# Kernel optimization log

Hardware: AMD Instinct MI355X
Metric: run time of the kernel (lower is better)

Reference implementation:

```python
import jax, jax.numpy as jnp
import numpy as np

N = 50000   # nodes per graph
E = 800000  # edges per graph
D = 128     # in_dim (num_features)
H = 128     # hidden_channels
R = 8       # num_etypes


def setup_inputs() -> dict:
    key = jax.random.key(0)
    ks = jax.random.split(key, 32)
    inp = {}
    inp["x1"] = jax.random.normal(ks[0], (N, D), dtype=jnp.float32)
    inp["edge_index1"] = jax.random.randint(ks[1], (2, E), 0, N)
    inp["edge_type1"] = jnp.sort(jax.random.randint(ks[2], (E,), 0, R))
    inp["x2"] = jax.random.normal(ks[3], (N, D), dtype=jnp.float32)
    inp["edge_index2"] = jax.random.randint(ks[4], (2, E), 0, N)
    inp["edge_type2"] = jnp.sort(jax.random.randint(ks[5], (E,), 0, R))
    # RGCNConv params: relation weights [R, in, out], root weight [in, out], bias [out]
    dims = [(D, H), (H, H), (H, H)]
    k = 6
    for l, (di, do) in enumerate(dims):
        s = 1.0 / np.sqrt(di)
        inp[f"W{l}"] = jax.random.normal(ks[k], (R, di, do), dtype=jnp.float32) * s; k += 1
        inp[f"root{l}"] = jax.random.normal(ks[k], (di, do), dtype=jnp.float32) * s; k += 1
        inp[f"bias{l}"] = jnp.zeros((do,), dtype=jnp.float32)
    # FCL: MLP on concat(u1, u2) of width 2*H -> H -> 1 (assumed architecture)
    s = 1.0 / np.sqrt(2 * H)
    inp["fc1_w"] = jax.random.normal(ks[k], (2 * H, H), dtype=jnp.float32) * s; k += 1
    inp["fc1_b"] = jnp.zeros((H,), dtype=jnp.float32)
    s = 1.0 / np.sqrt(H)
    inp["fc2_w"] = jax.random.normal(ks[k], (H, 1), dtype=jnp.float32) * s; k += 1
    inp["fc2_b"] = jnp.zeros((1,), dtype=jnp.float32)
    return inp


def rgcn_conv(x, src, dst, etype, W, root, bias):
    # PyG RGCNConv: out_i = root @ x_i + bias + sum_r mean_{j in N_r(i)} W_r x_j
    # transform all nodes by all relation weights: [R, N, H]
    t = jnp.einsum('nd,rdh->rnh', x, W)
    msg = t[etype, src]                       # [E, H] per-edge gathered messages
    comb = dst * R + etype                    # combined (node, relation) segment id
    cnt = jax.ops.segment_sum(jnp.ones((E,), x.dtype), comb, num_segments=N * R)
    msg = msg * (1.0 / jnp.maximum(cnt, 1.0))[comb][:, None]  # per-relation mean norm
    agg = jax.ops.segment_sum(msg, dst, num_segments=N)       # scatter-add over relations
    return agg + x @ root + bias


def gnn(x, edge_index, edge_type, params):
    src, dst = edge_index[0], edge_index[1]
    u = jax.nn.relu(rgcn_conv(x, src, dst, edge_type, *params[0]))
    u = jax.nn.relu(rgcn_conv(u, src, dst, edge_type, *params[1]))
    u = rgcn_conv(u, src, dst, edge_type, *params[2])
    return jnp.mean(u, axis=0).reshape(1, -1)  # [1, H]


def reference(x1, edge_index1, edge_type1, x2, edge_index2, edge_type2,
              W0, root0, bias0, W1, root1, bias1, W2, root2, bias2,
              fc1_w, fc1_b, fc2_w, fc2_b):
    params = [(W0, root0, bias0), (W1, root1, bias1), (W2, root2, bias2)]
    u1 = gnn(x1, edge_index1, edge_type1, params)
    u2 = gnn(x2, edge_index2, edge_type2, params)
    h = jnp.concatenate([u1, u2], axis=-1)    # [1, 2H]
    return jax.nn.relu(h @ fc1_w + fc1_b) @ fc2_w + fc2_b  # [1, 1]
```

## Files before the change

kernel.cpp:

```cpp
#include <hip/hip_runtime.h>

#define R_ET 8
#define DH 128

typedef __bf16 bf16x8 __attribute__((ext_vector_type(8)));
typedef float f32x4 __attribute__((ext_vector_type(4)));

__device__ __forceinline__ ushort f2bf(float f) {
  unsigned u = __float_as_uint(f);
  u += 0x7fff + ((u >> 16) & 1);
  return (ushort)(u >> 16);
}


__global__ void count_kernel(const int* __restrict__ ei, const int* __restrict__ et,
                             int* __restrict__ cnt, int E) {
  int e = blockIdx.x * blockDim.x + threadIdx.x;
  if (e < E) atomicAdd(&cnt[ei[E + e] * R_ET + et[e]], 1);
}

__global__ __launch_bounds__(1024) void scan1_kernel(const int* __restrict__ cnt,
                                                     int* __restrict__ off,
                                                     int* __restrict__ bsum, int N) {
  __shared__ int s[1024];
  int tid = threadIdx.x;
  int node = blockIdx.x * 1024 + tid;
  int d = 0;
  if (node < N) {
    const int4* c = (const int4*)&cnt[node * R_ET];
    int4 a = c[0], b = c[1];
    d = a.x + a.y + a.z + a.w + b.x + b.y + b.z + b.w;
  }
  s[tid] = d;
  __syncthreads();
  for (int step = 1; step < 1024; step <<= 1) {
    int v = (tid >= step) ? s[tid - step] : 0;
    __syncthreads();
    s[tid] += v;
    __syncthreads();
  }
  if (node < N) off[node] = s[tid] - d;
  if (tid == 1023) bsum[blockIdx.x] = s[1023];
}

__global__ __launch_bounds__(1024) void scan2_kernel(int* __restrict__ bsum, int nb) {
  __shared__ int s[1024];
  int tid = threadIdx.x;
  int v = (tid < nb) ? bsum[tid] : 0;
  s[tid] = v;
  __syncthreads();
  for (int step = 1; step < 1024; step <<= 1) {
    int x = (tid >= step) ? s[tid - step] : 0;
    __syncthreads();
    s[tid] += x;
    __syncthreads();
  }
  if (tid < nb) bsum[tid] = s[tid] - v;
}

__global__ __launch_bounds__(1024) void scan3_kernel(int* __restrict__ off,
                                                     int* __restrict__ cursor,
                                                     const int* __restrict__ bsum,
                                                     int N, int E) {
  int node = blockIdx.x * 1024 + threadIdx.x;
  if (node < N) {
    int o = off[node] + bsum[blockIdx.x];
    off[node] = o;
    cursor[node] = o;
  }
  if (node == 0) off[N] = E;
}

__global__ void place_kernel(const int* __restrict__ ei, const int* __restrict__ et,
                             const int* __restrict__ cnt, int* __restrict__ cursor,
                             int2* __restrict__ meta, int E) {
  int e = blockIdx.x * blockDim.x + threadIdx.x;
  if (e >= E) return;
  int src = ei[e], dst = ei[E + e], r = et[e];
  int slot = atomicAdd(&cursor[dst], 1);
  meta[slot] = make_int2(src | (r << 28),
                         __float_as_int(1.f / (float)cnt[dst * R_ET + r]));
}

__global__ __launch_bounds__(256) void wconv_kernel(const float* __restrict__ root,
                                                    const float* __restrict__ W,
                                                    ushort* __restrict__ Wt) {
  int mat = blockIdx.x;
  const float* src = (mat == 0) ? root : (W + (size_t)(mat - 1) * DH * DH);
  ushort* dst = Wt + (size_t)mat * DH * DH;
  for (int idx = threadIdx.x; idx < DH * DH; idx += 256) {
    int n = idx >> 7, k = idx & 127;
    dst[n * DH + (((k >> 3) ^ (n & 7)) << 3) + (k & 7)] = f2bf(src[k * DH + n]);
  }
}

__global__ __launch_bounds__(256) void aconv_kernel(const float* __restrict__ src,
                                                    ushort* __restrict__ dst,
                                                    int total, int padtotal) {
  int i4 = (blockIdx.x * 256 + threadIdx.x) * 4;
  if (i4 >= padtotal) return;
  int row = i4 >> 7, k = i4 & 127;
  ushort4 o = make_ushort4(0, 0, 0, 0);
  if (i4 < total) {
    float4 v = *(const float4*)&src[i4];
    o = make_ushort4(f2bf(v.x), f2bf(v.y), f2bf(v.z), f2bf(v.w));
  }
  *(ushort4*)&dst[(size_t)row * DH + (((k >> 3) ^ (row & 7)) << 3) + (k & 7)] = o;
}

__global__ __launch_bounds__(256) void gemm_mfma(
    const ushort* __restrict__ Abf, const ushort* __restrict__ Wt,
    const float* __restrict__ bias, float* __restrict__ y,
    ushort* __restrict__ t, int N) {
  __shared__ ushort As[128 * DH];
  __shared__ ushort Bs[128 * DH];
  const int tid = threadIdx.x;
  const int wave = tid >> 6, lane = tid & 63;
  const int quad = lane >> 4, l15 = lane & 15;
  const int rbase = blockIdx.x * 128;
  const int wr = (wave >> 1) * 64, wc = (wave & 1) * 64;

  const ushort* gA = Abf + (size_t)rbase * DH;
#pragma unroll
  for (int it = 0; it < 8; it++) {
    __builtin_amdgcn_global_load_lds(
        (const __attribute__((address_space(1))) void*)(gA + (it * 256 + tid) * 8),
        (__attribute__((address_space(3))) void*)(As + (it * 256 + wave * 64) * 8), 16, 0, 0);
  }

  for (int m = 0; m < 3; m++) {
    const int mat = blockIdx.y * 3 + m;
    const ushort* gB = Wt + (size_t)mat * DH * DH;
    if (m) __syncthreads();
#pragma unroll
    for (int it = 0; it < 8; it++) {
      __builtin_amdgcn_global_load_lds(
          (const __attribute__((address_space(1))) void*)(gB + (it * 256 + tid) * 8),
          (__attribute__((address_space(3))) void*)(Bs + (it * 256 + wave * 64) * 8), 16, 0, 0);
    }
    __syncthreads();

    f32x4 acc[4][4];
#pragma unroll
    for (int i = 0; i < 4; i++)
#pragma unroll
      for (int j = 0; j < 4; j++) acc[i][j] = (f32x4){0.f, 0.f, 0.f, 0.f};

#pragma unroll
    for (int kc = 0; kc < 4; kc++) {
      bf16x8 af[4], bfr[4];
#pragma unroll
      for (int i = 0; i < 4; i++) {
        int ra = wr + i * 16 + l15;
        int rb = wc + i * 16 + l15;
        af[i] = *(const bf16x8*)&As[ra * DH + (((kc * 4 + quad) ^ (ra & 7)) << 3)];
        bfr[i] = *(const bf16x8*)&Bs[rb * DH + (((kc * 4 + quad) ^ (rb & 7)) << 3)];
      }
#pragma unroll
      for (int i = 0; i < 4; i++)
#pragma unroll
        for (int j = 0; j < 4; j++)
          acc[i][j] = __builtin_amdgcn_mfma_f32_16x16x32_bf16(af[i], bfr[j], acc[i][j], 0, 0, 0);
    }

    if (mat == 0) {
#pragma unroll
      for (int j = 0; j < 4; j++) {
        int col = wc + j * 16 + l15;
        float bv = bias[col];
#pragma unroll
        for (int i = 0; i < 4; i++)
#pragma unroll
          for (int r = 0; r < 4; r++) {
            int row = rbase + wr + i * 16 + quad * 4 + r;
            if (row < N) y[(size_t)row * DH + col] = acc[i][j][r] + bv;
          }
      }
    } else {
      ushort* tp = t + (size_t)(mat - 1) * N * DH;
#pragma unroll
      for (int j = 0; j < 4; j++) {
        int col = wc + j * 16 + l15;
#pragma unroll
        for (int i = 0; i < 4; i++)
#pragma unroll
          for (int r = 0; r < 4; r++) {
            int row = rbase + wr + i * 16 + quad * 4 + r;
            if (row < N) tp[(size_t)row * DH + col] = f2bf(acc[i][j][r]);
          }
      }
    }
  }
}

__device__ __forceinline__ void gather_accum(const int2* __restrict__ meta,
                                             const ushort* __restrict__ t,
                                             int start, int end, int lane, int N,
                                             float& ax, float& ay) {
  const int colb = lane * 2;
  for (int base = start; base < end; base += 64) {
    int m = min(64, end - base);
    int2 md = make_int2(0, 0);
    if (lane < m) md = meta[base + lane];
    int j = 0;
    for (; j + 4 <= m; j += 4) {
      int p0 = __shfl(md.x, j),     q0 = __shfl(md.y, j);
      int p1 = __shfl(md.x, j + 1), q1 = __shfl(md.y, j + 1);
      int p2 = __shfl(md.x, j + 2), q2 = __shfl(md.y, j + 2);
      int p3 = __shfl(md.x, j + 3), q3 = __shfl(md.y, j + 3);
      unsigned u0 = *(const unsigned*)&t[(((size_t)((unsigned)p0 >> 28) * N + (p0 & 0x0fffffff)) << 7) + colb];
      unsigned u1 = *(const unsigned*)&t[(((size_t)((unsigned)p1 >> 28) * N + (p1 & 0x0fffffff)) << 7) + colb];
      unsigned u2 = *(const unsigned*)&t[(((size_t)((unsigned)p2 >> 28) * N + (p2 & 0x0fffffff)) << 7) + colb];
      unsigned u3 = *(const unsigned*)&t[(((size_t)((unsigned)p3 >> 28) * N + (p3 & 0x0fffffff)) << 7) + colb];
      float s0 = __int_as_float(q0), s1 = __int_as_float(q1);
      float s2 = __int_as_float(q2), s3 = __int_as_float(q3);
      ax = fmaf(__uint_as_float(u0 << 16), s0, ax);
      ay = fmaf(__uint_as_float(u0 & 0xffff0000u), s0, ay);
      ax = fmaf(__uint_as_float(u1 << 16), s1, ax);
      ay = fmaf(__uint_as_float(u1 & 0xffff0000u), s1, ay);
      ax = fmaf(__uint_as_float(u2 << 16), s2, ax);
      ay = fmaf(__uint_as_float(u2 & 0xffff0000u), s2, ay);
      ax = fmaf(__uint_as_float(u3 << 16), s3, ax);
      ay = fmaf(__uint_as_float(u3 & 0xffff0000u), s3, ay);
    }
    for (; j < m; j++) {
      int pj = __shfl(md.x, j);
      float sj = __int_as_float(__shfl(md.y, j));
      unsigned u = *(const unsigned*)&t[(((size_t)((unsigned)pj >> 28) * N + (pj & 0x0fffffff)) << 7) + colb];
      ax = fmaf(__uint_as_float(u << 16), sj, ax);
      ay = fmaf(__uint_as_float(u & 0xffff0000u), sj, ay);
    }
  }
}

__global__ __launch_bounds__(256) void gather_mid(
    const int* __restrict__ off, const int2* __restrict__ meta,
    const ushort* __restrict__ t, const float* __restrict__ y,
    ushort* __restrict__ Abf, int N) {
  int dst = blockIdx.x * 4 + (threadIdx.x >> 6);
  if (dst >= N) return;
  int lane = threadIdx.x & 63;
  float ax = 0.f, ay = 0.f;
  gather_accum(meta, t, off[dst], off[dst + 1], lane, N, ax, ay);
  float2 yv = *(const float2*)&y[(size_t)dst * DH + lane * 2];
  float rx = fmaxf(yv.x + ax, 0.f);
  float ry = fmaxf(yv.y + ay, 0.f);
  unsigned o = (unsigned)f2bf(rx) | ((unsigned)f2bf(ry) << 16);
  int k = lane * 2;
  *(unsigned*)&Abf[(size_t)dst * DH + (((k >> 3) ^ (dst & 7)) << 3) + (k & 7)] = o;
}

__global__ __launch_bounds__(256) void gather_last(
    const int* __restrict__ off, const int2* __restrict__ meta,
    const ushort* __restrict__ t, float* __restrict__ y, int N) {
  int dst = blockIdx.x * 4 + (threadIdx.x >> 6);
  if (dst >= N) return;
  int lane = threadIdx.x & 63;
  float ax = 0.f, ay = 0.f;
  gather_accum(meta, t, off[dst], off[dst + 1], lane, N, ax, ay);
  float2* yp = (float2*)&y[(size_t)dst * DH + lane * 2];
  float2 yv = *yp;
  yv.x += ax;
  yv.y += ay;
  *yp = yv;
}

__global__ __launch_bounds__(256) void pool_kernel(const float* __restrict__ y,
                                                   float* __restrict__ u, int N) {
  __shared__ float s[256];
  int tid = threadIdx.x;
  int c = tid & 127, rr = tid >> 7;
  int n0 = blockIdx.x * 100;
  int nend = min(n0 + 100, N);
  float sum = 0.f;
  for (int n = n0 + rr; n < nend; n += 2) sum += y[(size_t)n * DH + c];
  s[tid] = sum;
  __syncthreads();
  if (tid < 128) atomicAdd(&u[c], s[tid] + s[tid + 128]);
}

__global__ __launch_bounds__(256) void mlp_kernel(
    const float* __restrict__ u, const float* __restrict__ fc1w,
    const float* __restrict__ fc1b, const float* __restrict__ fc2w,
    const float* __restrict__ fc2b, float* __restrict__ out, int N) {
  __shared__ float uin[256];
  __shared__ float hred[128];
  int tid = threadIdx.x;
  uin[tid] = u[tid] * (1.f / (float)N);
  __syncthreads();
  if (tid < 128) {
    float s = fc1b[tid];
    for (int i = 0; i < 256; i++) s = fmaf(uin[i], fc1w[i * 128 + tid], s);
    s = fmaxf(s, 0.f);
    hred[tid] = s * fc2w[tid];
  }
  __syncthreads();
  if (tid == 0) {
    float s = fc2b[0];
    for (int i = 0; i < 128; i++) s += hred[i];
    out[0] = s;
  }
}

extern "C" void kernel_launch(void* const* d_in, const int* in_sizes, int n_in,
                              void* d_out, int out_size, void* d_ws, size_t ws_size,
                              hipStream_t stream) {
  const float* x[2] = {(const float*)d_in[0], (const float*)d_in[3]};
  const int* ei[2] = {(const int*)d_in[1], (const int*)d_in[4]};
  const int* et[2] = {(const int*)d_in[2], (const int*)d_in[5]};
  const float* Wp[3] = {(const float*)d_in[6], (const float*)d_in[9], (const float*)d_in[12]};
  const float* rootp[3] = {(const float*)d_in[7], (const float*)d_in[10], (const float*)d_in[13]};
  const float* biasp[3] = {(const float*)d_in[8], (const float*)d_in[11], (const float*)d_in[14]};
  const float* fc1w = (const float*)d_in[15];
  const float* fc1b = (const float*)d_in[16];
  const float* fc2w = (const float*)d_in[17];
  const float* fc2b = (const float*)d_in[18];

  const int N = in_sizes[0] / DH;
  const int E = in_sizes[2];
  const int Npad = (N + 127) & ~127;
  const int NB = (N + 1023) / 1024;

  char* ws = (char*)d_ws;
  size_t ob = 0;
  auto alloc = [&](size_t bytes) {
    void* p = ws + ob;
    ob = (ob + bytes + 255) & ~(size_t)255;
    return p;
  };
  float* y = (float*)alloc((size_t)N * DH * 4);
  int* cnt = (int*)alloc((size_t)N * R_ET * 4);
  int* offs = (int*)alloc((size_t)(N + 1) * 4);
  int* cursor = (int*)alloc((size_t)N * 4);
  int* bsum = (int*)alloc(1024 * 4);
  int2* meta = (int2*)alloc((size_t)E * 8);
  float* u = (float*)alloc(1024);
  ushort* Abf = (ushort*)alloc((size_t)Npad * DH * 2);
  ushort* Wt = (ushort*)alloc((size_t)3 * 9 * DH * DH * 2);
  ushort* tbuf = (ushort*)alloc((size_t)R_ET * N * DH * 2);
  (void)ws_size;

  hipMemsetAsync(u, 0, 2 * DH * sizeof(float), stream);
  for (int l = 0; l < 3; l++)
    wconv_kernel<<<9, 256, 0, stream>>>(rootp[l], Wp[l], Wt + (size_t)l * 9 * DH * DH);

  dim3 ggrid(Npad / 128, 3);
  dim3 egrid((E + 255) / 256);
  dim3 ngrid((N + 3) / 4);
  const int total = N * DH, padtotal = Npad * DH;
  dim3 agrid((padtotal / 4 + 255) / 256);

  for (int g = 0; g < 2; g++) {
    hipMemsetAsync(cnt, 0, (size_t)N * R_ET * sizeof(int), stream);
    count_kernel<<<egrid, 256, 0, stream>>>(ei[g], et[g], cnt, E);
    scan1_kernel<<<NB, 1024, 0, stream>>>(cnt, offs, bsum, N);
    scan2_kernel<<<1, 1024, 0, stream>>>(bsum, NB);
    scan3_kernel<<<NB, 1024, 0, stream>>>(offs, cursor, bsum, N, E);
    place_kernel<<<egrid, 256, 0, stream>>>(ei[g], et[g], cnt, cursor, meta, E);
    aconv_kernel<<<agrid, 256, 0, stream>>>(x[g], Abf, total, padtotal);
    for (int l = 0; l < 3; l++) {
      gemm_mfma<<<ggrid, 256, 0, stream>>>(Abf, Wt + (size_t)l * 9 * DH * DH,
                                           biasp[l], y, tbuf, N);
      if (l < 2) {
        gather_mid<<<ngrid, 256, 0, stream>>>(offs, meta, tbuf, y, Abf, N);
      } else {
        gather_last<<<ngrid, 256, 0, stream>>>(offs, meta, tbuf, y, N);
      }
    }
    pool_kernel<<<(N + 99) / 100, 256, 0, stream>>>(y, u + g * DH, N);
  }
  mlp_kernel<<<1, 256, 0, stream>>>(u, fc1w, fc1b, fc2w, fc2b, (float*)d_out, N);
}
```

Measured before the change: 887.6 us.

## Sort edges by (dst, relation), shrink edge metadata, fuse pooling and staged GEMM stores

The CSR is now built over (node, relation) segments, so per-edge metadata shrinks to a single int. The mean normalization is computed per destination from the counts and broadcast by shuffle. The root transform goes into a ninth bf16 slab instead of an fp32 y buffer. GEMM output is staged through LDS for coalesced 16-byte stores. The final gather fuses mean pooling with atomic adds, which removes the pool kernel and the fp32 y traffic, and the last-layer bias is folded into the MLP. In exchange, the scan now runs over an 8x larger segment array, and the root path is stored in bf16, which adds rounding error.

```diff
diff --git a/kernel.cpp b/kernel.cpp
--- a/kernel.cpp
+++ b/kernel.cpp
@@ -5,6 +5,7 @@
 
 typedef __bf16 bf16x8 __attribute__((ext_vector_type(8)));
 typedef float f32x4 __attribute__((ext_vector_type(4)));
+typedef ushort u16x8 __attribute__((ext_vector_type(8)));
 
 __device__ __forceinline__ ushort f2bf(float f) {
   unsigned u = __float_as_uint(f);
@@ -12,7 +13,6 @@
   return (ushort)(u >> 16);
 }
 
-
 __global__ void count_kernel(const int* __restrict__ ei, const int* __restrict__ et,
                              int* __restrict__ cnt, int E) {
   int e = blockIdx.x * blockDim.x + threadIdx.x;
@@ -21,16 +21,11 @@
 
 __global__ __launch_bounds__(1024) void scan1_kernel(const int* __restrict__ cnt,
                                                      int* __restrict__ off,
-                                                     int* __restrict__ bsum, int N) {
+                                                     int* __restrict__ bsum, int M) {
   __shared__ int s[1024];
   int tid = threadIdx.x;
-  int node = blockIdx.x * 1024 + tid;
-  int d = 0;
-  if (node < N) {
-    const int4* c = (const int4*)&cnt[node * R_ET];
-    int4 a = c[0], b = c[1];
-    d = a.x + a.y + a.z + a.w + b.x + b.y + b.z + b.w;
-  }
+  int i = blockIdx.x * 1024 + tid;
+  int d = (i < M) ? cnt[i] : 0;
   s[tid] = d;
   __syncthreads();
   for (int step = 1; step < 1024; step <<= 1) {
@@ -39,7 +34,7 @@
     s[tid] += v;
     __syncthreads();
   }
-  if (node < N) off[node] = s[tid] - d;
+  if (i < M) off[i] = s[tid] - d;
   if (tid == 1023) bsum[blockIdx.x] = s[1023];
 }
 
@@ -61,32 +56,30 @@
 __global__ __launch_bounds__(1024) void scan3_kernel(int* __restrict__ off,
                                                      int* __restrict__ cursor,
                                                      const int* __restrict__ bsum,
-                                                     int N, int E) {
-  int node = blockIdx.x * 1024 + threadIdx.x;
-  if (node < N) {
-    int o = off[node] + bsum[blockIdx.x];
-    off[node] = o;
-    cursor[node] = o;
-  }
-  if (node == 0) off[N] = E;
+                                                     int M, int E) {
+  int i = blockIdx.x * 1024 + threadIdx.x;
+  if (i < M) {
+    int o = off[i] + bsum[blockIdx.x];
+    off[i] = o;
+    cursor[i] = o;
+  }
+  if (i == 0) off[M] = E;
 }
 
 __global__ void place_kernel(const int* __restrict__ ei, const int* __restrict__ et,
-                             const int* __restrict__ cnt, int* __restrict__ cursor,
-                             int2* __restrict__ meta, int E) {
+                             int* __restrict__ cursor, int* __restrict__ meta, int E) {
   int e = blockIdx.x * blockDim.x + threadIdx.x;
   if (e >= E) return;
   int src = ei[e], dst = ei[E + e], r = et[e];
-  int slot = atomicAdd(&cursor[dst], 1);
-  meta[slot] = make_int2(src | (r << 28),
-                         __float_as_int(1.f / (float)cnt[dst * R_ET + r]));
+  int slot = atomicAdd(&cursor[dst * R_ET + r], 1);
+  meta[slot] = src | (r << 28);
 }
 
 __global__ __launch_bounds__(256) void wconv_kernel(const float* __restrict__ root,
                                                     const float* __restrict__ W,
                                                     ushort* __restrict__ Wt) {
   int mat = blockIdx.x;
-  const float* src = (mat == 0) ? root : (W + (size_t)(mat - 1) * DH * DH);
+  const float* src = (mat == 8) ? root : (W + (size_t)mat * DH * DH);
   ushort* dst = Wt + (size_t)mat * DH * DH;
   for (int idx = threadIdx.x; idx < DH * DH; idx += 256) {
     int n = idx >> 7, k = idx & 127;
@@ -110,8 +103,7 @@
 
 __global__ __launch_bounds__(256) void gemm_mfma(
     const ushort* __restrict__ Abf, const ushort* __restrict__ Wt,
-    const float* __restrict__ bias, float* __restrict__ y,
-    ushort* __restrict__ t, int N) {
+    ushort* __restrict__ t, int Npad) {
   __shared__ ushort As[128 * DH];
   __shared__ ushort Bs[128 * DH];
   const int tid = threadIdx.x;
@@ -163,57 +155,46 @@
           acc[i][j] = __builtin_amdgcn_mfma_f32_16x16x32_bf16(af[i], bfr[j], acc[i][j], 0, 0, 0);
     }
 
-    if (mat == 0) {
+    __syncthreads();
+#pragma unroll
+    for (int i = 0; i < 4; i++)
 #pragma unroll
       for (int j = 0; j < 4; j++) {
         int col = wc + j * 16 + l15;
-        float bv = bias[col];
-#pragma unroll
-        for (int i = 0; i < 4; i++)
-#pragma unroll
-          for (int r = 0; r < 4; r++) {
-            int row = rbase + wr + i * 16 + quad * 4 + r;
-            if (row < N) y[(size_t)row * DH + col] = acc[i][j][r] + bv;
-          }
+#pragma unroll
+        for (int r = 0; r < 4; r++)
+          Bs[(wr + i * 16 + quad * 4 + r) * DH + col] = f2bf(acc[i][j][r]);
       }
-    } else {
-      ushort* tp = t + (size_t)(mat - 1) * N * DH;
-#pragma unroll
-      for (int j = 0; j < 4; j++) {
-        int col = wc + j * 16 + l15;
-#pragma unroll
-        for (int i = 0; i < 4; i++)
-#pragma unroll
-          for (int r = 0; r < 4; r++) {
-            int row = rbase + wr + i * 16 + quad * 4 + r;
-            if (row < N) tp[(size_t)row * DH + col] = f2bf(acc[i][j][r]);
-          }
-      }
-    }
-  }
-}
-
-__device__ __forceinline__ void gather_accum(const int2* __restrict__ meta,
+    __syncthreads();
+    ushort* tp = t + ((size_t)mat * Npad + rbase) * DH;
+#pragma unroll
+    for (int c = 0; c < 8; c++) {
+      u16x8 v = *(const u16x8*)&Bs[tid * 64 + c * 8];
+      *(u16x8*)&tp[tid * 64 + c * 8] = v;
+    }
+  }
+}
+
+__device__ __forceinline__ void gather_accum(const int* __restrict__ meta,
                                              const ushort* __restrict__ t,
-                                             int start, int end, int lane, int N,
+                                             int start, int end, int lane, int colb,
+                                             float invl, int NpadS,
                                              float& ax, float& ay) {
-  const int colb = lane * 2;
   for (int base = start; base < end; base += 64) {
     int m = min(64, end - base);
-    int2 md = make_int2(0, 0);
-    if (lane < m) md = meta[base + lane];
+    int md = (lane < m) ? meta[base + lane] : 0;
     int j = 0;
     for (; j + 4 <= m; j += 4) {
-      int p0 = __shfl(md.x, j),     q0 = __shfl(md.y, j);
-      int p1 = __shfl(md.x, j + 1), q1 = __shfl(md.y, j + 1);
-      int p2 = __shfl(md.x, j + 2), q2 = __shfl(md.y, j + 2);
-      int p3 = __shfl(md.x, j + 3), q3 = __shfl(md.y, j + 3);
-      unsigned u0 = *(const unsigned*)&t[(((size_t)((unsigned)p0 >> 28) * N + (p0 & 0x0fffffff)) << 7) + colb];
-      unsigned u1 = *(const unsigned*)&t[(((size_t)((unsigned)p1 >> 28) * N + (p1 & 0x0fffffff)) << 7) + colb];
-      unsigned u2 = *(const unsigned*)&t[(((size_t)((unsigned)p2 >> 28) * N + (p2 & 0x0fffffff)) << 7) + colb];
-      unsigned u3 = *(const unsigned*)&t[(((size_t)((unsigned)p3 >> 28) * N + (p3 & 0x0fffffff)) << 7) + colb];
-      float s0 = __int_as_float(q0), s1 = __int_as_float(q1);
-      float s2 = __int_as_float(q2), s3 = __int_as_float(q3);
+      int p0 = __shfl(md, j), p1 = __shfl(md, j + 1);
+      int p2 = __shfl(md, j + 2), p3 = __shfl(md, j + 3);
+      int r0 = (unsigned)p0 >> 28, r1 = (unsigned)p1 >> 28;
+      int r2 = (unsigned)p2 >> 28, r3 = (unsigned)p3 >> 28;
+      float s0 = __shfl(invl, r0), s1 = __shfl(invl, r1);
+      float s2 = __shfl(invl, r2), s3 = __shfl(invl, r3);
+      unsigned u0 = *(const unsigned*)&t[r0 * NpadS + ((p0 & 0x0fffffff) << 7) + colb];
+      unsigned u1 = *(const unsigned*)&t[r1 * NpadS + ((p1 & 0x0fffffff) << 7) + colb];
+      unsigned u2 = *(const unsigned*)&t[r2 * NpadS + ((p2 & 0x0fffffff) << 7) + colb];
+      unsigned u3 = *(const unsigned*)&t[r3 * NpadS + ((p3 & 0x0fffffff) << 7) + colb];
       ax = fmaf(__uint_as_float(u0 << 16), s0, ax);
       ay = fmaf(__uint_as_float(u0 & 0xffff0000u), s0, ay);
       ax = fmaf(__uint_as_float(u1 << 16), s1, ax);
@@ -224,9 +205,10 @@
       ay = fmaf(__uint_as_float(u3 & 0xffff0000u), s3, ay);
     }
     for (; j < m; j++) {
-      int pj = __shfl(md.x, j);
-      float sj = __int_as_float(__shfl(md.y, j));
-      unsigned u = *(const unsigned*)&t[(((size_t)((unsigned)pj >> 28) * N + (pj & 0x0fffffff)) << 7) + colb];
+      int pj = __shfl(md, j);
+      int rj = (unsigned)pj >> 28;
+      float sj = __shfl(invl, rj);
+      unsigned u = *(const unsigned*)&t[rj * NpadS + ((pj & 0x0fffffff) << 7) + colb];
       ax = fmaf(__uint_as_float(u << 16), sj, ax);
       ay = fmaf(__uint_as_float(u & 0xffff0000u), sj, ay);
     }
@@ -234,59 +216,64 @@
 }
 
 __global__ __launch_bounds__(256) void gather_mid(
-    const int* __restrict__ off, const int2* __restrict__ meta,
-    const ushort* __restrict__ t, const float* __restrict__ y,
-    ushort* __restrict__ Abf, int N) {
+    const int* __restrict__ off, const int* __restrict__ meta,
+    const int* __restrict__ cnt, const ushort* __restrict__ t,
+    const float* __restrict__ bias, ushort* __restrict__ Abf, int N, int Npad) {
   int dst = blockIdx.x * 4 + (threadIdx.x >> 6);
   if (dst >= N) return;
-  int lane = threadIdx.x & 63;
+  int lane = threadIdx.x & 63, colb = lane * 2;
+  int dst8 = dst * R_ET;
+  int NpadS = Npad * DH;
+  float invl = 1.f / (float)cnt[dst8 + (lane & 7)];
   float ax = 0.f, ay = 0.f;
-  gather_accum(meta, t, off[dst], off[dst + 1], lane, N, ax, ay);
-  float2 yv = *(const float2*)&y[(size_t)dst * DH + lane * 2];
-  float rx = fmaxf(yv.x + ax, 0.f);
-  float ry = fmaxf(yv.y + ay, 0.f);
+  gather_accum(meta, t, off[dst8], off[dst8 + 8], lane, colb, invl, NpadS, ax, ay);
+  unsigned u9 = *(const unsigned*)&t[8 * NpadS + (dst << 7) + colb];
+  float2 bv = *(const float2*)&bias[colb];
+  float rx = fmaxf(__uint_as_float(u9 << 16) + ax + bv.x, 0.f);
+  float ry = fmaxf(__uint_as_float(u9 & 0xffff0000u) + ay + bv.y, 0.f);
   unsigned o = (unsigned)f2bf(rx) | ((unsigned)f2bf(ry) << 16);
-  int k = lane * 2;
-  *(unsigned*)&Abf[(size_t)dst * DH + (((k >> 3) ^ (dst & 7)) << 3) + (k & 7)] = o;
+  *(unsigned*)&Abf[(size_t)dst * DH + (((colb >> 3) ^ (dst & 7)) << 3) + (colb & 7)] = o;
 }
 
 __global__ __launch_bounds__(256) void gather_last(
-    const int* __restrict__ off, const int2* __restrict__ meta,
-    const ushort* __restrict__ t, float* __restrict__ y, int N) {
-  int dst = blockIdx.x * 4 + (threadIdx.x >> 6);
-  if (dst >= N) return;
-  int lane = threadIdx.x & 63;
-  float ax = 0.f, ay = 0.f;
-  gather_accum(meta, t, off[dst], off[dst + 1], lane, N, ax, ay);
-  float2* yp = (float2*)&y[(size_t)dst * DH + lane * 2];
-  float2 yv = *yp;
-  yv.x += ax;
-  yv.y += ay;
-  *yp = yv;
-}
-
-__global__ __launch_bounds__(256) void pool_kernel(const float* __restrict__ y,
-                                                   float* __restrict__ u, int N) {
-  __shared__ float s[256];
-  int tid = threadIdx.x;
-  int c = tid & 127, rr = tid >> 7;
-  int n0 = blockIdx.x * 100;
-  int nend = min(n0 + 100, N);
-  float sum = 0.f;
-  for (int n = n0 + rr; n < nend; n += 2) sum += y[(size_t)n * DH + c];
-  s[tid] = sum;
-  __syncthreads();
-  if (tid < 128) atomicAdd(&u[c], s[tid] + s[tid + 128]);
+    const int* __restrict__ off, const int* __restrict__ meta,
+    const int* __restrict__ cnt, const ushort* __restrict__ t,
+    float* __restrict__ u, int N, int Npad) {
+  __shared__ float sx[256], sy[256];
+  int lane = threadIdx.x & 63, wave = threadIdx.x >> 6, colb = lane * 2;
+  int NpadS = Npad * DH;
+  float px = 0.f, py = 0.f;
+  for (int dd = 0; dd < 4; dd++) {
+    int dst = blockIdx.x * 16 + wave * 4 + dd;
+    if (dst >= N) break;
+    int dst8 = dst * R_ET;
+    float invl = 1.f / (float)cnt[dst8 + (lane & 7)];
+    float ax = 0.f, ay = 0.f;
+    gather_accum(meta, t, off[dst8], off[dst8 + 8], lane, colb, invl, NpadS, ax, ay);
+    unsigned u9 = *(const unsigned*)&t[8 * NpadS + (dst << 7) + colb];
+    px += __uint_as_float(u9 << 16) + ax;
+    py += __uint_as_float(u9 & 0xffff0000u) + ay;
+  }
+  sx[threadIdx.x] = px;
+  sy[threadIdx.x] = py;
+  __syncthreads();
+  if (threadIdx.x < 64) {
+    float tx = sx[threadIdx.x] + sx[64 + threadIdx.x] + sx[128 + threadIdx.x] + sx[192 + threadIdx.x];
+    float ty = sy[threadIdx.x] + sy[64 + threadIdx.x] + sy[128 + threadIdx.x] + sy[192 + threadIdx.x];
+    atomicAdd(&u[threadIdx.x * 2], tx);
+    atomicAdd(&u[threadIdx.x * 2 + 1], ty);
+  }
 }
 
 __global__ __launch_bounds__(256) void mlp_kernel(
-    const float* __restrict__ u, const float* __restrict__ fc1w,
-    const float* __restrict__ fc1b, const float* __restrict__ fc2w,
-    const float* __restrict__ fc2b, float* __restrict__ out, int N) {
+    const float* __restrict__ u, const float* __restrict__ bias2,
+    const float* __restrict__ fc1w, const float* __restrict__ fc1b,
+    const float* __restrict__ fc2w, const float* __restrict__ fc2b,
+    float* __restrict__ out, int N) {
   __shared__ float uin[256];
   __shared__ float hred[128];
   int tid = threadIdx.x;
-  uin[tid] = u[tid] * (1.f / (float)N);
+  uin[tid] = u[tid] * (1.f / (float)N) + bias2[tid & 127];
   __syncthreads();
   if (tid < 128) {
     float s = fc1b[tid];
@@ -319,7 +306,8 @@
   const int N = in_sizes[0] / DH;
   const int E = in_sizes[2];
   const int Npad = (N + 127) & ~127;
-  const int NB = (N + 1023) / 1024;
+  const int M = N * R_ET;
+  const int MB = (M + 1023) / 1024;
 
   char* ws = (char*)d_ws;
   size_t ob = 0;
@@ -328,16 +316,15 @@
     ob = (ob + bytes + 255) & ~(size_t)255;
     return p;
   };
-  float* y = (float*)alloc((size_t)N * DH * 4);
-  int* cnt = (int*)alloc((size_t)N * R_ET * 4);
-  int* offs = (int*)alloc((size_t)(N + 1) * 4);
-  int* cursor = (int*)alloc((size_t)N * 4);
+  int* cnt = (int*)alloc((size_t)M * 4);
+  int* offs = (int*)alloc((size_t)(M + 1) * 4);
+  int* cursor = (int*)alloc((size_t)M * 4);
   int* bsum = (int*)alloc(1024 * 4);
-  int2* meta = (int2*)alloc((size_t)E * 8);
+  int* meta = (int*)alloc((size_t)E * 4);
   float* u = (float*)alloc(1024);
   ushort* Abf = (ushort*)alloc((size_t)Npad * DH * 2);
   ushort* Wt = (ushort*)alloc((size_t)3 * 9 * DH * DH * 2);
-  ushort* tbuf = (ushort*)alloc((size_t)R_ET * N * DH * 2);
+  ushort* tbuf = (ushort*)alloc((size_t)9 * Npad * DH * 2);
   (void)ws_size;
 
   hipMemsetAsync(u, 0, 2 * DH * sizeof(float), stream);
@@ -346,28 +333,28 @@
 
   dim3 ggrid(Npad / 128, 3);
   dim3 egrid((E + 255) / 256);
-  dim3 ngrid((N + 3) / 4);
   const int total = N * DH, padtotal = Npad * DH;
   dim3 agrid((padtotal / 4 + 255) / 256);
 
   for (int g = 0; g < 2; g++) {
-    hipMemsetAsync(cnt, 0, (size_t)N * R_ET * sizeof(int), stream);
+    hipMemsetAsync(cnt, 0, (size_t)M * sizeof(int), stream);
     count_kernel<<<egrid, 256, 0, stream>>>(ei[g], et[g], cnt, E);
-    scan1_kernel<<<NB, 1024, 0, stream>>>(cnt, offs, bsum, N);
-    scan2_kernel<<<1, 1024, 0, stream>>>(bsum, NB);
-    scan3_kernel<<<NB, 1024, 0, stream>>>(offs, cursor, bsum, N, E);
-    place_kernel<<<egrid, 256, 0, stream>>>(ei[g], et[g], cnt, cursor, meta, E);
+    scan1_kernel<<<MB, 1024, 0, stream>>>(cnt, offs, bsum, M);
+    scan2_kernel<<<1, 1024, 0, stream>>>(bsum, MB);
+    scan3_kernel<<<MB, 1024, 0, stream>>>(offs, cursor, bsum, M, E);
+    place_kernel<<<egrid, 256, 0, stream>>>(ei[g], et[g], cursor, meta, E);
     aconv_kernel<<<agrid, 256, 0, stream>>>(x[g], Abf, total, padtotal);
     for (int l = 0; l < 3; l++) {
-      gemm_mfma<<<ggrid, 256, 0, stream>>>(Abf, Wt + (size_t)l * 9 * DH * DH,
-                                           biasp[l], y, tbuf, N);
+      gemm_mfma<<<ggrid, 256, 0, stream>>>(Abf, Wt + (size_t)l * 9 * DH * DH, tbuf, Npad);
       if (l < 2) {
-        gather_mid<<<ngrid, 256, 0, stream>>>(offs, meta, tbuf, y, Abf, N);
+        gather_mid<<<(N + 3) / 4, 256, 0, stream>>>(offs, meta, cnt, tbuf, biasp[l],
+                                                    Abf, N, Npad);
       } else {
-        gather_last<<<ngrid, 256, 0, stream>>>(offs, meta, tbuf, y, N);
+        gather_last<<<(N + 15) / 16, 256, 0, stream>>>(offs, meta, cnt, tbuf,
+                                                       u + g * DH, N, Npad);
       }
     }
-    pool_kernel<<<(N + 99) / 100, 256, 0, stream>>>(y, u + g * DH, N);
-  }
-  mlp_kernel<<<1, 256, 0, stream>>>(u, fc1w, fc1b, fc2w, fc2b, (float*)d_out, N);
-}
+  }
+  mlp_kernel<<<1, 256, 0, stream>>>(u, biasp[2], fc1w, fc1b, fc2w, fc2b,
+                                    (float*)d_out, N);
+}
```

After: 1.186 ms. 1.34x slower.
